# Optimization experiments

Measured on AMD Instinct MI355X. Metric: run time of the kernel, lower is better.

Reference implementation:

```python
import jax, jax.numpy as jnp
import numpy as np

B, T, HID = 2, 2048, 2048
NH, NKV = 16, 8
NOPE, ROPE = 128, 64
HD = NOPE + ROPE  # 192
VD = 128
KV_RANK, Q_RANK = 512, 1536
EPS = 1e-6
THETA = 10000.0
GROUPS = NH // NKV


def rmsnorm(x, w):
    var = jnp.mean(x * x, axis=-1, keepdims=True)
    return x * jax.lax.rsqrt(var + EPS) * w


def rope_cos_sin(seq_len, dtype):
    inv_freq = 1.0 / (THETA ** (jnp.arange(0, ROPE, 2, dtype=jnp.float32) / ROPE))
    t = jnp.arange(seq_len, dtype=jnp.float32)
    freqs = jnp.outer(t, inv_freq)
    emb = jnp.concatenate([freqs, freqs], axis=-1)  # [T, ROPE]
    return jnp.cos(emb).astype(dtype)[None, :, None, :], jnp.sin(emb).astype(dtype)[None, :, None, :]


def rotate_half(x):
    x1, x2 = x[..., : x.shape[-1] // 2], x[..., x.shape[-1] // 2 :]
    return jnp.concatenate([-x2, x1], axis=-1)


def setup_inputs() -> dict:
    key = jax.random.key(0)
    ks = jax.random.split(key, 7)
    s = 0.02
    return {
        "hidden_states": jax.random.normal(ks[0], (B, T, HID), jnp.float32),
        "q_a_w": jax.random.normal(ks[1], (HID, Q_RANK), jnp.float32) * s,
        "q_a_ln_w": jnp.ones((Q_RANK,), jnp.float32),
        "q_b_w": jax.random.normal(ks[2], (Q_RANK, NH * HD), jnp.float32) * s,
        "kv_a_w": jax.random.normal(ks[3], (HID, KV_RANK + NKV * ROPE), jnp.float32) * s,
        "kv_a_ln_w": jnp.ones((KV_RANK,), jnp.float32),
        "kv_b_w": jax.random.normal(ks[4], (KV_RANK, NKV * (NOPE + VD)), jnp.float32) * s,
        "o_w": jax.random.normal(ks[5], (NH * VD, HID), jnp.float32) * s,
    }


def reference(hidden_states, q_a_w, q_a_ln_w, q_b_w, kv_a_w, kv_a_ln_w, kv_b_w, o_w):
    x = hidden_states
    # Q low-rank path: a_proj -> RMSNorm -> b_proj
    q = rmsnorm(x @ q_a_w, q_a_ln_w) @ q_b_w
    q = q.reshape(B, T, NH, HD)
    q_nope, q_rope = q[..., :NOPE], q[..., NOPE:]
    # KV low-rank + decoupled rope key
    kv_raw = x @ kv_a_w
    kv_latent = rmsnorm(kv_raw[..., :KV_RANK], kv_a_ln_w)
    k_rope = kv_raw[..., KV_RANK:].reshape(B, T, NKV, ROPE)
    kv = (kv_latent @ kv_b_w).reshape(B, T, NKV, NOPE + VD)
    k_nope, v = kv[..., :NOPE], kv[..., NOPE:]
    # partial RoPE on rope slice only
    cos, sin = rope_cos_sin(T, x.dtype)
    q_rope = q_rope * cos + rotate_half(q_rope) * sin
    k_rope = k_rope * cos + rotate_half(k_rope) * sin
    q_full = jnp.concatenate([q_nope, q_rope], axis=-1)  # [B,T,NH,HD]
    k_full = jnp.concatenate([k_nope, k_rope], axis=-1)  # [B,T,NKV,HD]
    # GQA expansion (repeat_interleave over head dim)
    k_full = jnp.repeat(k_full, GROUPS, axis=2)  # [B,T,NH,HD]
    v_full = jnp.repeat(v, GROUPS, axis=2)       # [B,T,NH,VD]
    scale = HD ** -0.5
    scores = jnp.einsum("bqhd,bkhd->bhqk", q_full, k_full) * scale
    probs = jax.nn.softmax(scores, axis=-1)
    attn = jnp.einsum("bhqk,bkhd->bqhd", probs, v_full)
    out = attn.reshape(B, T, NH * VD) @ o_w
    return out
```

## Files before the change

kernel.cpp:

```cpp
#include <hip/hip_runtime.h>

using u16 = unsigned short;
using u32 = unsigned int;

typedef float f32x4 __attribute__((ext_vector_type(4)));
typedef __bf16 bf16x8 __attribute__((ext_vector_type(8)));

__device__ __forceinline__ u16 f2bf(float f){
  u32 u = __builtin_bit_cast(u32, f);
  u32 r = (u + 0x7fffu + ((u >> 16) & 1u)) >> 16;
  return (u16)r;
}
__device__ __forceinline__ float bf2f(u16 h){
  u32 u = ((u32)h) << 16;
  return __builtin_bit_cast(float, u);
}
__device__ __forceinline__ void gl2lds16(const void* g, void* l){
  __builtin_amdgcn_global_load_lds((const __attribute__((address_space(1))) u32*)g,
                                   (__attribute__((address_space(3))) u32*)l, 16, 0, 0);
}
__device__ __forceinline__ int swz24(int ck, int r){ return (ck & 24) | ((ck ^ r) & 7); }
__device__ __forceinline__ u32 cvtpk_bf16(float a, float b){
  u32 r; asm("v_cvt_pk_bf16_f32 %0, %1, %2" : "=v"(r) : "v"(a), "v"(b)); return r;
}

__global__ __launch_bounds__(256) void cvt_f32_bf16(const float* __restrict__ in,
                                                    u16* __restrict__ out, long n){
  long i = ((long)blockIdx.x*256 + threadIdx.x)*4;
  if (i >= n) return;
  float4 v = *(const float4*)(in + i);
  u16 o[4] = { f2bf(v.x), f2bf(v.y), f2bf(v.z), f2bf(v.w) };
  *(ushort4*)(out + i) = *(ushort4*)o;
}

__global__ __launch_bounds__(256) void transpose_w(const float* __restrict__ in,
                                                   u16* __restrict__ out, int K, int N){
  __shared__ float tile[32][33];
  int n0 = blockIdx.x*32, k0 = blockIdx.y*32;
  int tx = threadIdx.x, ty = threadIdx.y;
  for (int i = ty; i < 32; i += 8)
    tile[i][tx] = in[(size_t)(k0+i)*N + n0+tx];
  __syncthreads();
  for (int i = ty; i < 32; i += 8)
    out[(size_t)(n0+i)*K + k0+tx] = f2bf(tile[tx][i]);
}

__global__ __launch_bounds__(256) void rope_tables(float* __restrict__ cosT, float* __restrict__ sinT){
  int idx = blockIdx.x*256 + threadIdx.x;
  int t = idx >> 5, d = idx & 31;
  double inv = pow(10000.0, -(double)d / 32.0);
  double a = (double)t * inv;
  cosT[idx] = (float)cos(a);
  sinT[idx] = (float)sin(a);
}

__device__ __forceinline__ void remap_block(int NX, int& bx, int& by){
  int id = blockIdx.y*NX + blockIdx.x;
  bx = id >> 5;
  by = ((id & 7) << 2) | ((id >> 3) & 3);
}

template<int OUT_BF16>
__global__ __launch_bounds__(256) void gemm_bt(const u16* __restrict__ A,
                                               const u16* __restrict__ Bt,
                                               void* __restrict__ Cout,
                                               int M, int N, int K, float cscale){
  __shared__ u16 As[128*32];
  __shared__ u16 Bs[128*32];
  const int tid = threadIdx.x, lane = tid & 63, wave = tid >> 6;
  int bx, by; remap_block(gridDim.x, bx, by);
  const int m0 = by*128, n0 = bx*128;
  const int wm = (wave >> 1)*64, wn = (wave & 1)*64;
  const int g = lane >> 4, lr = lane & 15;
  f32x4 acc[4][4] = {};
  const int sr = (wave*2)*16 + (lane >> 2);
  const int sc = (lane & 3)*8;
  for (int k0 = 0; k0 < K; k0 += 32){
    __syncthreads();
    #pragma unroll
    for (int i = 0; i < 2; i++){
      int c = wave*2 + i;
      int r = sr + i*16;
      gl2lds16(A  + (size_t)(m0+r)*K + k0 + sc, (char*)As + c*1024);
      gl2lds16(Bt + (size_t)(n0+r)*K + k0 + sc, (char*)Bs + c*1024);
    }
    __syncthreads();
    bf16x8 af[4], bfr[4];
    #pragma unroll
    for (int mi = 0; mi < 4; mi++) af[mi]  = *reinterpret_cast<const bf16x8*>(&As[(wm+mi*16+lr)*32 + g*8]);
    #pragma unroll
    for (int ni = 0; ni < 4; ni++) bfr[ni] = *reinterpret_cast<const bf16x8*>(&Bs[(wn+ni*16+lr)*32 + g*8]);
    #pragma unroll
    for (int mi = 0; mi < 4; mi++)
      #pragma unroll
      for (int ni = 0; ni < 4; ni++)
        acc[mi][ni] = __builtin_amdgcn_mfma_f32_16x16x32_bf16(af[mi], bfr[ni], acc[mi][ni], 0,0,0);
  }
  #pragma unroll
  for (int mi = 0; mi < 4; mi++)
    #pragma unroll
    for (int ni = 0; ni < 4; ni++)
      #pragma unroll
      for (int r = 0; r < 4; r++){
        int row = m0 + wm + mi*16 + g*4 + r;
        int col = n0 + wn + ni*16 + lr;
        float v = acc[mi][ni][r];
        if (OUT_BF16) ((u16*)Cout)[(size_t)row*N + col] = f2bf(v*cscale);
        else          ((float*)Cout)[(size_t)row*N + col] = v;
      }
}

__global__ __launch_bounds__(256) void gemm_qb_rope(const u16* __restrict__ A,
                                                    const u16* __restrict__ Bt,
                                                    u16* __restrict__ C,
                                                    const float* __restrict__ cosT,
                                                    const float* __restrict__ sinT){
  constexpr int N = 3072, K = 1536;
  constexpr float qscale = 0.07216878364870322f;
  __shared__ u16 As[128*32];
  __shared__ u16 Bs[128*32];
  const int tid = threadIdx.x, lane = tid & 63, wave = tid >> 6;
  int bx, by; remap_block(gridDim.x, bx, by);
  const int m0 = by*128, n0 = bx*128;
  const int wm = (wave >> 1)*64, wn = (wave & 1)*64;
  const int g = lane >> 4, lr = lane & 15;
  f32x4 acc[4][4] = {};
  const int sr = (wave*2)*16 + (lane >> 2);
  const int sc = (lane & 3)*8;
  for (int k0 = 0; k0 < K; k0 += 32){
    __syncthreads();
    #pragma unroll
    for (int i = 0; i < 2; i++){
      int c = wave*2 + i;
      int r = sr + i*16;
      gl2lds16(A  + (size_t)(m0+r)*K + k0 + sc, (char*)As + c*1024);
      gl2lds16(Bt + (size_t)(n0+r)*K + k0 + sc, (char*)Bs + c*1024);
    }
    __syncthreads();
    bf16x8 af[4], bfr[4];
    #pragma unroll
    for (int mi = 0; mi < 4; mi++) af[mi]  = *reinterpret_cast<const bf16x8*>(&As[(wm+mi*16+lr)*32 + g*8]);
    #pragma unroll
    for (int ni = 0; ni < 4; ni++) bfr[ni] = *reinterpret_cast<const bf16x8*>(&Bs[(wn+ni*16+lr)*32 + g*8]);
    #pragma unroll
    for (int mi = 0; mi < 4; mi++)
      #pragma unroll
      for (int ni = 0; ni < 4; ni++)
        acc[mi][ni] = __builtin_amdgcn_mfma_f32_16x16x32_bf16(af[mi], bfr[ni], acc[mi][ni], 0,0,0);
  }
  const bool rope = (((n0 + wn) >> 6) % 3) == 2;
  #pragma unroll
  for (int mi = 0; mi < 4; mi++)
    #pragma unroll
    for (int r = 0; r < 4; r++){
      int row = m0 + wm + mi*16 + g*4 + r;
      int t = row & 2047;
      u16* crow = C + (size_t)row*N + n0 + wn;
      if (rope){
        #pragma unroll
        for (int np = 0; np < 2; np++){
          int dp = np*16 + lr;
          float x1 = acc[mi][np][r]*qscale, x2 = acc[mi][np+2][r]*qscale;
          float cv = cosT[t*32 + dp], sv = sinT[t*32 + dp];
          crow[dp]      = f2bf(x1*cv - x2*sv);
          crow[dp + 32] = f2bf(x2*cv + x1*sv);
        }
      } else {
        #pragma unroll
        for (int ni = 0; ni < 4; ni++)
          crow[ni*16 + lr] = f2bf(acc[mi][ni][r]*qscale);
      }
    }
}

__global__ __launch_bounds__(256) void rmsnorm_bf16(const u16* __restrict__ in,
                                                    const float* __restrict__ w,
                                                    u16* __restrict__ out, int ncols, int instride){
  int row = blockIdx.x;
  const u16* x = in + (size_t)row*instride;
  int c = threadIdx.x;
  float xs[8];
  float ss = 0.f;
  int nch = ncols >> 3;
  if (c < nch){
    ushort4 a = *(const ushort4*)(x + c*8);
    ushort4 bq = *(const ushort4*)(x + c*8 + 4);
    u16 e[8] = {a.x,a.y,a.z,a.w,bq.x,bq.y,bq.z,bq.w};
    #pragma unroll
    for (int j = 0; j < 8; j++){ xs[j] = bf2f(e[j]); ss += xs[j]*xs[j]; }
  }
  #pragma unroll
  for (int m = 1; m < 64; m <<= 1) ss += __shfl_xor(ss, m, 64);
  __shared__ float p[4];
  if ((threadIdx.x & 63) == 0) p[threadIdx.x >> 6] = ss;
  __syncthreads();
  float inv = rsqrtf((p[0]+p[1]+p[2]+p[3]) / (float)ncols + 1e-6f);
  if (c < nch){
    u16 o[8];
    #pragma unroll
    for (int j = 0; j < 8; j++) o[j] = f2bf(xs[j]*inv*w[c*8+j]);
    *(ushort4*)(out + (size_t)row*ncols + c*8)     = *(ushort4*)o;
    *(ushort4*)(out + (size_t)row*ncols + c*8 + 4) = *(ushort4*)(o+4);
  }
}

__global__ __launch_bounds__(256) void kv_split_kernel(const u16* __restrict__ kvraw,
                                                       const float* __restrict__ lnw,
                                                       const float* __restrict__ cosT,
                                                       const float* __restrict__ sinT,
                                                       u16* __restrict__ kvlat,
                                                       u16* __restrict__ Kf){
  int row = blockIdx.x;
  int t = row & 2047, b = row >> 11;
  const u16* x = kvraw + (size_t)row*2560 + 1536;
  int c = threadIdx.x;
  float xs[4];
  float ss = 0.f;
  if (c < 128){
    ushort4 a = *(const ushort4*)(x + c*4);
    u16 e[4] = {a.x,a.y,a.z,a.w};
    #pragma unroll
    for (int j = 0; j < 4; j++){ xs[j] = bf2f(e[j]); ss += xs[j]*xs[j]; }
  }
  #pragma unroll
  for (int m = 1; m < 64; m <<= 1) ss += __shfl_xor(ss, m, 64);
  __shared__ float p[4];
  if ((threadIdx.x & 63) == 0) p[threadIdx.x >> 6] = ss;
  __syncthreads();
  float inv = rsqrtf((p[0]+p[1]+p[2]+p[3]) / 512.0f + 1e-6f);
  if (c < 128){
    u16 o[4];
    #pragma unroll
    for (int j = 0; j < 4; j++) o[j] = f2bf(xs[j]*inv*lnw[c*4+j]);
    *(ushort4*)(kvlat + (size_t)row*512 + c*4) = *(ushort4*)o;
  }
  int kh = threadIdx.x >> 5, dp = threadIdx.x & 31;
  float x1 = bf2f(x[512 + kh*64 + dp]), x2 = bf2f(x[512 + kh*64 + dp + 32]);
  float cv = cosT[t*32 + dp], sv = sinT[t*32 + dp];
  float o1 = x1*cv - x2*sv;
  float o2 = x2*cv + x1*sv;
  u16* kr = Kf + ((size_t)(b*8 + kh)*2048 + t)*192;
  int c1 = 128 + dp, c2 = 128 + dp + 32;
  kr[(swz24(c1 >> 3, t) << 3) | (c1 & 7)] = f2bf(o1);
  kr[(swz24(c2 >> 3, t) << 3) | (c2 & 7)] = f2bf(o2);
}

__global__ __launch_bounds__(256) void kv_rearrange(const u16* __restrict__ kv,
                                                    u16* __restrict__ vT,
                                                    u16* __restrict__ Kf){
  int bid = blockIdx.x;
  int tt = bid & 31, kvh = (bid >> 5) & 7, b = bid >> 8;
  int t0 = tt*64;
  __shared__ u16 tile[64][136];
  int tid = threadIdx.x;
  #pragma unroll
  for (int i = 0; i < 4; i++){
    int c2 = tid + i*256;
    int rr = c2 >> 4, ck = c2 & 15;
    int t = t0 + rr;
    int ck2 = (ck & 8) | ((ck ^ t) & 7);
    uint4 v = *(const uint4*)(kv + ((size_t)(b*2048 + t))*2048 + kvh*256 + ck*8);
    *(uint4*)(Kf + ((size_t)(b*8 + kvh)*2048 + t)*192 + ck2*8) = v;
  }
  #pragma unroll
  for (int i = 0; i < 4; i++){
    int c = tid + i*256;
    int r = c >> 4, ck = c & 15;
    const u16* src = kv + ((size_t)(b*2048 + t0 + r))*2048 + kvh*256 + 128 + ck*8;
    *(uint4*)&tile[r][ck*8] = *(const uint4*)src;
  }
  __syncthreads();
  #pragma unroll
  for (int i = 0; i < 4; i++){
    int c = tid + i*256;
    int vd = c >> 3, tc = c & 7;
    int stc = tc ^ (vd & 7);
    uint4 tv;
    u16* tp = (u16*)&tv;
    #pragma unroll
    for (int j = 0; j < 8; j++) tp[j] = tile[tc*8 + j][vd];
    *(uint4*)(vT + ((size_t)(b*8 + kvh)*128 + vd)*2048 + t0 + stc*8) = tv;
  }
}

__global__ __launch_bounds__(256, 2) void attn_kernel(const u16* __restrict__ Q,
                                                      const u16* __restrict__ Kf,
                                                      const u16* __restrict__ Vt,
                                                      u16* __restrict__ Oa){
  constexpr int T = 2048;
  constexpr int NT = T/64;
  __shared__ u16 Ks[64*192];
  __shared__ u16 Vs[2][128*64];
  __shared__ u16 Ps[4][2048];
  const int tid = threadIdx.x, lane = tid & 63, wave = tid >> 6;
  const int g = lane >> 4, lr = lane & 15;

  const int wg = blockIdx.x;
  const int role = (wg & 7)*64 + (wg >> 3);
  const int grp = role >> 5;
  const int b = grp >> 3, kvh = grp & 7;
  const int within = role & 31;
  const int h = kvh*2 + (within >> 4);
  const int q0 = (within & 15)*128 + wave*32;

  bf16x8 aq[2][6];
  #pragma unroll
  for (int qg = 0; qg < 2; qg++){
    const u16* qrow = Q + ((size_t)b*T + q0 + qg*16 + lr)*3072 + h*192;
    #pragma unroll
    for (int kc = 0; kc < 6; kc++)
      aq[qg][kc] = *reinterpret_cast<const bf16x8*>(qrow + kc*32 + g*8);
  }
  const u16* Kbase = Kf + (size_t)(b*8 + kvh)*T*192;
  const u16* Vbase = Vt + (size_t)(b*8 + kvh)*128*T;

  f32x4 ovb[2][8] = {};
  float mq[2] = {-1e30f, -1e30f};
  float lq[2] = {0.f, 0.f};

  auto stageK = [&](int kt){
    const u16* ksrc = Kbase + (size_t)kt*12288 + wave*3072 + lane*8;
    #pragma unroll
    for (int i = 0; i < 6; i++)
      gl2lds16(ksrc + i*512, (char*)Ks + (wave*6 + i)*1024);
  };
  auto stageV = [&](int kt, int buf){
    #pragma unroll
    for (int i = 0; i < 4; i++){
      int c = wave*4 + i;
      const u16* vsrc = Vbase + (size_t)(c*8 + (lane >> 3))*T + kt*64 + (lane & 7)*8;
      gl2lds16(vsrc, (char*)(&Vs[0][0]) + buf*16384 + c*1024);
    }
  };

  stageK(0);
  stageV(0, 0);
  __syncthreads();

  int buf = 0;
  for (int kt = 0; kt < NT; kt++){
    const bool notlast = (kt + 1 < NT);
    if (notlast) stageV(kt + 1, buf ^ 1);

    f32x4 s[2][4];
    __builtin_amdgcn_s_setprio(1);
    #pragma unroll
    for (int nb = 0; nb < 4; nb++){
      const int row = nb*16 + lr;
      f32x4 a0 = {0.f,0.f,0.f,0.f}, a1 = {0.f,0.f,0.f,0.f};
      #pragma unroll
      for (int kc = 0; kc < 6; kc++){
        int ckl = swz24(kc*4 + g, row);
        bf16x8 kf = *reinterpret_cast<const bf16x8*>(&Ks[row*192 + ckl*8]);
        a0 = __builtin_amdgcn_mfma_f32_16x16x32_bf16(kf, aq[0][kc], a0, 0,0,0);
        a1 = __builtin_amdgcn_mfma_f32_16x16x32_bf16(kf, aq[1][kc], a1, 0,0,0);
      }
      s[0][nb] = a0; s[1][nb] = a1;
    }
    __builtin_amdgcn_s_setprio(0);

    asm volatile("s_waitcnt lgkmcnt(0)" ::: "memory");
    __builtin_amdgcn_s_barrier();
    __builtin_amdgcn_sched_barrier(0);
    if (notlast) stageK(kt + 1);

    #pragma unroll
    for (int qg = 0; qg < 2; qg++){
      float pm = s[qg][0][0];
      #pragma unroll
      for (int nb = 0; nb < 4; nb++)
        #pragma unroll
        for (int r = 0; r < 4; r++)
          if (nb || r) pm = fmaxf(pm, s[qg][nb][r]);
      pm = fmaxf(pm, __shfl_xor(pm, 16, 64));
      pm = fmaxf(pm, __shfl_xor(pm, 32, 64));
      if (!__all(pm <= mq[qg] + 8.f)){
        float mn = fmaxf(mq[qg], pm);
        float corr = __expf(mq[qg] - mn);
        mq[qg] = mn;
        lq[qg] *= corr;
        #pragma unroll
        for (int r = 0; r < 4; r++){
          float cr = __shfl(corr, (lane & 48) | (g*4 + r), 64);
          #pragma unroll
          for (int vb = 0; vb < 8; vb++) ovb[qg][vb][r] *= cr;
        }
      }
      float ls = 0.f;
      #pragma unroll
      for (int nb = 0; nb < 4; nb++){
        float e0 = __expf(s[qg][nb][0] - mq[qg]);
        float e1 = __expf(s[qg][nb][1] - mq[qg]);
        float e2 = __expf(s[qg][nb][2] - mq[qg]);
        float e3 = __expf(s[qg][nb][3] - mq[qg]);
        ls += (e0 + e1) + (e2 + e3);
        int stc = (2*nb + (g >> 1)) ^ (lr & 7);
        volatile u32* p = (volatile u32*)&Ps[wave][qg*1024 + lr*64 + stc*8 + (g & 1)*4];
        p[0] = cvtpk_bf16(e0, e1);
        p[1] = cvtpk_bf16(e2, e3);
      }
      ls += __shfl_xor(ls, 16, 64);
      ls += __shfl_xor(ls, 32, 64);
      lq[qg] += ls;
    }

    asm volatile("s_waitcnt lgkmcnt(0)" ::: "memory");
    __builtin_amdgcn_sched_barrier(0);

    bf16x8 ap[2][2];
    #pragma unroll
    for (int qg = 0; qg < 2; qg++)
      #pragma unroll
      for (int k2 = 0; k2 < 2; k2++){
        int ck = (k2*4 + g) ^ (lr & 7);
        ap[qg][k2] = *reinterpret_cast<const bf16x8*>(&Ps[wave][qg*1024 + lr*64 + ck*8]);
      }
    __builtin_amdgcn_s_setprio(1);
    #pragma unroll
    for (int vb = 0; vb < 8; vb++)
      #pragma unroll
      for (int k2 = 0; k2 < 2; k2++){
        int vd = vb*16 + lr;
        int ck = (k2*4 + g) ^ (vd & 7);
        bf16x8 bv = *reinterpret_cast<const bf16x8*>(&Vs[buf][vd*64 + ck*8]);
        ovb[0][vb] = __builtin_amdgcn_mfma_f32_16x16x32_bf16(ap[0][k2], bv, ovb[0][vb], 0,0,0);
        ovb[1][vb] = __builtin_amdgcn_mfma_f32_16x16x32_bf16(ap[1][k2], bv, ovb[1][vb], 0,0,0);
      }
    __builtin_amdgcn_s_setprio(0);

    if (notlast) __syncthreads();
    buf ^= 1;
  }

  #pragma unroll
  for (int qg = 0; qg < 2; qg++){
    float invq = 1.0f / lq[qg];
    float inv_r[4];
    #pragma unroll
    for (int r = 0; r < 4; r++)
      inv_r[r] = __shfl(invq, (lane & 48) | (g*4 + r), 64);
    u16* obase = Oa + ((size_t)b*T + q0 + qg*16)*2048 + h*128;
    #pragma unroll
    for (int vb = 0; vb < 8; vb++)
      #pragma unroll
      for (int r = 0; r < 4; r++)
        obase[(size_t)(g*4 + r)*2048 + vb*16 + lr] = f2bf(ovb[qg][vb][r]*inv_r[r]);
  }
}

extern "C" void kernel_launch(void* const* d_in, const int* in_sizes, int n_in,
                              void* d_out, int out_size, void* d_ws, size_t ws_size,
                              hipStream_t stream){
  const float* hs      = (const float*)d_in[0];
  const float* q_a_w   = (const float*)d_in[1];
  const float* q_a_ln  = (const float*)d_in[2];
  const float* q_b_w   = (const float*)d_in[3];
  const float* kv_a_w  = (const float*)d_in[4];
  const float* kv_a_ln = (const float*)d_in[5];
  const float* kv_b_w  = (const float*)d_in[6];
  const float* o_w     = (const float*)d_in[7];

  char* ws = (char*)d_ws;
  size_t off = 0;
  auto alloc = [&](size_t bytes){ void* p = ws + off; off += bytes; return p; };
  u16*  Wqa   = (u16*)alloc(1536ull*2048*2);
  u16*  Wkva  = (u16*)alloc(1024ull*2048*2);
  u16*  Wqb   = (u16*)alloc(3072ull*1536*2);
  u16*  Wkvb  = (u16*)alloc(2048ull*512*2);
  u16*  Wo    = (u16*)alloc(2048ull*2048*2);
  u16*  XB    = (u16*)alloc(4096ull*2048*2);
  u16*  R23   = (u16*)alloc(4096ull*2560*2);
  u16*  QB    = (u16*)alloc(4096ull*3072*2);
  u16*  Qlat  = (u16*)alloc(4096ull*1536*2);
  u16*  KVlat = (u16*)alloc(4096ull*512*2);
  u16*  Kf    = (u16*)alloc(2ull*8*2048*192*2);
  u16*  Vt    = (u16*)alloc(2ull*8*128*2048*2);
  float* cosT = (float*)alloc(2048ull*32*4);
  float* sinT = (float*)alloc(2048ull*32*4);
  (void)ws_size; (void)in_sizes; (void)n_in; (void)out_size;

  u16* KVB = R23;

  cvt_f32_bf16<<<8192, 256, 0, stream>>>(hs, XB, 4096ll*2048);
  transpose_w<<<dim3(1536/32, 2048/32), dim3(32,8), 0, stream>>>(q_a_w,  Wqa,  2048, 1536);
  transpose_w<<<dim3(1024/32, 2048/32), dim3(32,8), 0, stream>>>(kv_a_w, Wkva, 2048, 1024);
  transpose_w<<<dim3(3072/32, 1536/32), dim3(32,8), 0, stream>>>(q_b_w,  Wqb,  1536, 3072);
  transpose_w<<<dim3(2048/32,  512/32), dim3(32,8), 0, stream>>>(kv_b_w, Wkvb,  512, 2048);
  transpose_w<<<dim3(2048/32, 2048/32), dim3(32,8), 0, stream>>>(o_w,    Wo,   2048, 2048);
  rope_tables<<<256, 256, 0, stream>>>(cosT, sinT);

  gemm_bt<1><<<dim3(20, 32), 256, 0, stream>>>(XB, Wqa, R23, 4096, 2560, 2048, 1.0f);
  rmsnorm_bf16<<<4096, 256, 0, stream>>>(R23, q_a_ln, Qlat, 1536, 2560);
  kv_split_kernel<<<4096, 256, 0, stream>>>(R23, kv_a_ln, cosT, sinT, KVlat, Kf);
  gemm_qb_rope<<<dim3(24, 32), 256, 0, stream>>>(Qlat, Wqb, QB, cosT, sinT);
  gemm_bt<1><<<dim3(16, 32), 256, 0, stream>>>(KVlat, Wkvb, KVB, 4096, 2048, 512, 1.0f);
  kv_rearrange<<<512, 256, 0, stream>>>(KVB, Vt, Kf);
  attn_kernel<<<512, 256, 0, stream>>>(QB, Kf, Vt, XB);
  gemm_bt<0><<<dim3(16, 32), 256, 0, stream>>>(XB, Wo, (float*)d_out, 4096, 2048, 2048, 1.0f);
}
```

Measured before the change: 348.5 us.

## Pass P via shuffles, single-buffer V, use exp2 with folded log2e, raise occupancy

The attention kernel stops staging softmax probabilities through LDS and builds the MFMA A-operands with cross-lane shuffles instead. It drops the V double buffer, so V for the next tile is loaded only after a barrier at the end of each iteration. The freed LDS allows launch bounds of three blocks per SM. log2(e) is folded into the Q scale so exp2f can replace __expf, and the row-sum reduction is deferred to the epilogue. The risk is that V load latency is now exposed and the shuffle work may cost more than the LDS round trip it replaces.

```diff
diff --git a/kernel.cpp b/kernel.cpp
--- a/kernel.cpp
+++ b/kernel.cpp
@@ -5,6 +5,7 @@
 
 typedef float f32x4 __attribute__((ext_vector_type(4)));
 typedef __bf16 bf16x8 __attribute__((ext_vector_type(8)));
+typedef u32 u32x4 __attribute__((ext_vector_type(4)));
 
 __device__ __forceinline__ u16 f2bf(float f){
   u32 u = __builtin_bit_cast(u32, f);
@@ -116,7 +117,7 @@
                                                     const float* __restrict__ cosT,
                                                     const float* __restrict__ sinT){
   constexpr int N = 3072, K = 1536;
-  constexpr float qscale = 0.07216878364870322f;
+  constexpr float qscale = 0.07216878364870322f * 1.44269504088896340f;
   __shared__ u16 As[128*32];
   __shared__ u16 Bs[128*32];
   const int tid = threadIdx.x, lane = tid & 63, wave = tid >> 6;
@@ -283,15 +284,14 @@
   }
 }
 
-__global__ __launch_bounds__(256, 2) void attn_kernel(const u16* __restrict__ Q,
+__global__ __launch_bounds__(256, 3) void attn_kernel(const u16* __restrict__ Q,
                                                       const u16* __restrict__ Kf,
                                                       const u16* __restrict__ Vt,
                                                       u16* __restrict__ Oa){
   constexpr int T = 2048;
   constexpr int NT = T/64;
   __shared__ u16 Ks[64*192];
-  __shared__ u16 Vs[2][128*64];
-  __shared__ u16 Ps[4][2048];
+  __shared__ u16 Vs[128*64];
   const int tid = threadIdx.x, lane = tid & 63, wave = tid >> 6;
   const int g = lane >> 4, lr = lane & 15;
 
@@ -324,23 +324,21 @@
     for (int i = 0; i < 6; i++)
       gl2lds16(ksrc + i*512, (char*)Ks + (wave*6 + i)*1024);
   };
-  auto stageV = [&](int kt, int buf){
+  auto stageV = [&](int kt){
     #pragma unroll
     for (int i = 0; i < 4; i++){
       int c = wave*4 + i;
       const u16* vsrc = Vbase + (size_t)(c*8 + (lane >> 3))*T + kt*64 + (lane & 7)*8;
-      gl2lds16(vsrc, (char*)(&Vs[0][0]) + buf*16384 + c*1024);
+      gl2lds16(vsrc, (char*)Vs + c*1024);
     }
   };
 
   stageK(0);
-  stageV(0, 0);
+  stageV(0);
   __syncthreads();
 
-  int buf = 0;
   for (int kt = 0; kt < NT; kt++){
     const bool notlast = (kt + 1 < NT);
-    if (notlast) stageV(kt + 1, buf ^ 1);
 
     f32x4 s[2][4];
     __builtin_amdgcn_s_setprio(1);
@@ -359,11 +357,10 @@
     }
     __builtin_amdgcn_s_setprio(0);
 
-    asm volatile("s_waitcnt lgkmcnt(0)" ::: "memory");
-    __builtin_amdgcn_s_barrier();
-    __builtin_amdgcn_sched_barrier(0);
+    __syncthreads();
     if (notlast) stageK(kt + 1);
 
+    u32 pk[2][4][2];
     #pragma unroll
     for (int qg = 0; qg < 2; qg++){
       float pm = s[qg][0][0];
@@ -376,7 +373,7 @@
       pm = fmaxf(pm, __shfl_xor(pm, 32, 64));
       if (!__all(pm <= mq[qg] + 8.f)){
         float mn = fmaxf(mq[qg], pm);
-        float corr = __expf(mq[qg] - mn);
+        float corr = exp2f(mq[qg] - mn);
         mq[qg] = mn;
         lq[qg] *= corr;
         #pragma unroll
@@ -389,52 +386,64 @@
       float ls = 0.f;
       #pragma unroll
       for (int nb = 0; nb < 4; nb++){
-        float e0 = __expf(s[qg][nb][0] - mq[qg]);
-        float e1 = __expf(s[qg][nb][1] - mq[qg]);
-        float e2 = __expf(s[qg][nb][2] - mq[qg]);
-        float e3 = __expf(s[qg][nb][3] - mq[qg]);
+        float e0 = exp2f(s[qg][nb][0] - mq[qg]);
+        float e1 = exp2f(s[qg][nb][1] - mq[qg]);
+        float e2 = exp2f(s[qg][nb][2] - mq[qg]);
+        float e3 = exp2f(s[qg][nb][3] - mq[qg]);
         ls += (e0 + e1) + (e2 + e3);
-        int stc = (2*nb + (g >> 1)) ^ (lr & 7);
-        volatile u32* p = (volatile u32*)&Ps[wave][qg*1024 + lr*64 + stc*8 + (g & 1)*4];
-        p[0] = cvtpk_bf16(e0, e1);
-        p[1] = cvtpk_bf16(e2, e3);
-      }
-      ls += __shfl_xor(ls, 16, 64);
-      ls += __shfl_xor(ls, 32, 64);
+        pk[qg][nb][0] = cvtpk_bf16(e0, e1);
+        pk[qg][nb][1] = cvtpk_bf16(e2, e3);
+      }
       lq[qg] += ls;
     }
 
-    asm volatile("s_waitcnt lgkmcnt(0)" ::: "memory");
-    __builtin_amdgcn_sched_barrier(0);
-
-    bf16x8 ap[2][2];
-    #pragma unroll
-    for (int qg = 0; qg < 2; qg++)
-      #pragma unroll
-      for (int k2 = 0; k2 < 2; k2++){
-        int ck = (k2*4 + g) ^ (lr & 7);
-        ap[qg][k2] = *reinterpret_cast<const bf16x8*>(&Ps[wave][qg*1024 + lr*64 + ck*8]);
-      }
-    __builtin_amdgcn_s_setprio(1);
-    #pragma unroll
-    for (int vb = 0; vb < 8; vb++)
-      #pragma unroll
-      for (int k2 = 0; k2 < 2; k2++){
+    #pragma unroll
+    for (int c32 = 0; c32 < 2; c32++){
+      const int s0 = ((g & 1)*2)*16 + lr;
+      const int s1 = ((g & 1)*2 + 1)*16 + lr;
+      const int nbsel = g >> 1;
+      bf16x8 pa[2];
+      #pragma unroll
+      for (int qg = 0; qg < 2; qg++){
+        u32 a00 = (u32)__shfl((int)pk[qg][c32*2][0],   s0, 64);
+        u32 a01 = (u32)__shfl((int)pk[qg][c32*2][1],   s0, 64);
+        u32 a02 = (u32)__shfl((int)pk[qg][c32*2][0],   s1, 64);
+        u32 a03 = (u32)__shfl((int)pk[qg][c32*2][1],   s1, 64);
+        u32 a10 = (u32)__shfl((int)pk[qg][c32*2+1][0], s0, 64);
+        u32 a11 = (u32)__shfl((int)pk[qg][c32*2+1][1], s0, 64);
+        u32 a12 = (u32)__shfl((int)pk[qg][c32*2+1][0], s1, 64);
+        u32 a13 = (u32)__shfl((int)pk[qg][c32*2+1][1], s1, 64);
+        u32x4 av;
+        av.x = nbsel ? a10 : a00;
+        av.y = nbsel ? a11 : a01;
+        av.z = nbsel ? a12 : a02;
+        av.w = nbsel ? a13 : a03;
+        pa[qg] = __builtin_bit_cast(bf16x8, av);
+      }
+      __builtin_amdgcn_s_setprio(1);
+      #pragma unroll
+      for (int vb = 0; vb < 8; vb++){
         int vd = vb*16 + lr;
-        int ck = (k2*4 + g) ^ (vd & 7);
-        bf16x8 bv = *reinterpret_cast<const bf16x8*>(&Vs[buf][vd*64 + ck*8]);
-        ovb[0][vb] = __builtin_amdgcn_mfma_f32_16x16x32_bf16(ap[0][k2], bv, ovb[0][vb], 0,0,0);
-        ovb[1][vb] = __builtin_amdgcn_mfma_f32_16x16x32_bf16(ap[1][k2], bv, ovb[1][vb], 0,0,0);
-      }
-    __builtin_amdgcn_s_setprio(0);
-
-    if (notlast) __syncthreads();
-    buf ^= 1;
+        int ck = (c32*4 + g) ^ (vd & 7);
+        bf16x8 bv = *reinterpret_cast<const bf16x8*>(&Vs[vd*64 + ck*8]);
+        ovb[0][vb] = __builtin_amdgcn_mfma_f32_16x16x32_bf16(pa[0], bv, ovb[0][vb], 0,0,0);
+        ovb[1][vb] = __builtin_amdgcn_mfma_f32_16x16x32_bf16(pa[1], bv, ovb[1][vb], 0,0,0);
+      }
+      __builtin_amdgcn_s_setprio(0);
+    }
+
+    if (notlast){
+      __syncthreads();
+      stageV(kt + 1);
+    }
   }
 
   #pragma unroll
   for (int qg = 0; qg < 2; qg++){
-    float invq = 1.0f / lq[qg];
+    float lt = lq[qg];
+    lt += __shfl_xor(lt, 16, 64);
+    lt += __shfl_xor(lt, 32, 64);
+    float invq = 1.0f / lt;
     float inv_r[4];
     #pragma unroll
     for (int r = 0; r < 4; r++)
```

After: 432.5 us. 1.24x slower.

## Double-buffer GEMM LDS tiles and use exp2 softmax with deferred row-sum reduction

Applied to the files above, without the earlier changes.

The projection GEMMs now keep two LDS buffers, so the next K tile is fetched while the current one feeds the MFMAs, with one barrier per iteration instead of two. The attention softmax folds log2(e) into the Q scale so it can call exp2f instead of __expf. The cross-lane row-sum shuffles move out of the inner loop to a single reduction in the epilogue. The P-tile LDS swizzle also gains an extra XOR term meant to cut bank conflicts, at the cost of twice the LDS per GEMM block, which may lower occupancy.

```diff
diff --git a/kernel.cpp b/kernel.cpp
--- a/kernel.cpp
+++ b/kernel.cpp
@@ -65,8 +65,8 @@
                                                const u16* __restrict__ Bt,
                                                void* __restrict__ Cout,
                                                int M, int N, int K, float cscale){
-  __shared__ u16 As[128*32];
-  __shared__ u16 Bs[128*32];
+  __shared__ u16 As[2][128*32];
+  __shared__ u16 Bs[2][128*32];
   const int tid = threadIdx.x, lane = tid & 63, wave = tid >> 6;
   int bx, by; remap_block(gridDim.x, bx, by);
   const int m0 = by*128, n0 = bx*128;
@@ -75,26 +75,32 @@
   f32x4 acc[4][4] = {};
   const int sr = (wave*2)*16 + (lane >> 2);
   const int sc = (lane & 3)*8;
-  for (int k0 = 0; k0 < K; k0 += 32){
-    __syncthreads();
+  auto stage = [&](int k0, int bf){
     #pragma unroll
     for (int i = 0; i < 2; i++){
       int c = wave*2 + i;
       int r = sr + i*16;
-      gl2lds16(A  + (size_t)(m0+r)*K + k0 + sc, (char*)As + c*1024);
-      gl2lds16(Bt + (size_t)(n0+r)*K + k0 + sc, (char*)Bs + c*1024);
+      gl2lds16(A  + (size_t)(m0+r)*K + k0 + sc, (char*)(&As[bf][0]) + c*1024);
+      gl2lds16(Bt + (size_t)(n0+r)*K + k0 + sc, (char*)(&Bs[bf][0]) + c*1024);
     }
-    __syncthreads();
+  };
+  stage(0, 0);
+  __syncthreads();
+  int bf = 0;
+  for (int k0 = 0; k0 < K; k0 += 32){
+    if (k0 + 32 < K) stage(k0 + 32, bf ^ 1);
     bf16x8 af[4], bfr[4];
     #pragma unroll
-    for (int mi = 0; mi < 4; mi++) af[mi]  = *reinterpret_cast<const bf16x8*>(&As[(wm+mi*16+lr)*32 + g*8]);
-    #pragma unroll
-    for (int ni = 0; ni < 4; ni++) bfr[ni] = *reinterpret_cast<const bf16x8*>(&Bs[(wn+ni*16+lr)*32 + g*8]);
+    for (int mi = 0; mi < 4; mi++) af[mi]  = *reinterpret_cast<const bf16x8*>(&As[bf][(wm+mi*16+lr)*32 + g*8]);
+    #pragma unroll
+    for (int ni = 0; ni < 4; ni++) bfr[ni] = *reinterpret_cast<const bf16x8*>(&Bs[bf][(wn+ni*16+lr)*32 + g*8]);
     #pragma unroll
     for (int mi = 0; mi < 4; mi++)
       #pragma unroll
       for (int ni = 0; ni < 4; ni++)
         acc[mi][ni] = __builtin_amdgcn_mfma_f32_16x16x32_bf16(af[mi], bfr[ni], acc[mi][ni], 0,0,0);
+    __syncthreads();
+    bf ^= 1;
   }
   #pragma unroll
   for (int mi = 0; mi < 4; mi++)
@@ -116,9 +122,9 @@
                                                     const float* __restrict__ cosT,
                                                     const float* __restrict__ sinT){
   constexpr int N = 3072, K = 1536;
-  constexpr float qscale = 0.07216878364870322f;
-  __shared__ u16 As[128*32];
-  __shared__ u16 Bs[128*32];
+  constexpr float qscale = 0.07216878364870322f * 1.44269504088896340f;
+  __shared__ u16 As[2][128*32];
+  __shared__ u16 Bs[2][128*32];
   const int tid = threadIdx.x, lane = tid & 63, wave = tid >> 6;
   int bx, by; remap_block(gridDim.x, bx, by);
   const int m0 = by*128, n0 = bx*128;
@@ -127,26 +133,32 @@
   f32x4 acc[4][4] = {};
   const int sr = (wave*2)*16 + (lane >> 2);
   const int sc = (lane & 3)*8;
-  for (int k0 = 0; k0 < K; k0 += 32){
-    __syncthreads();
+  auto stage = [&](int k0, int bf){
     #pragma unroll
     for (int i = 0; i < 2; i++){
       int c = wave*2 + i;
       int r = sr + i*16;
-      gl2lds16(A  + (size_t)(m0+r)*K + k0 + sc, (char*)As + c*1024);
-      gl2lds16(Bt + (size_t)(n0+r)*K + k0 + sc, (char*)Bs + c*1024);
+      gl2lds16(A  + (size_t)(m0+r)*K + k0 + sc, (char*)(&As[bf][0]) + c*1024);
+      gl2lds16(Bt + (size_t)(n0+r)*K + k0 + sc, (char*)(&Bs[bf][0]) + c*1024);
     }
-    __syncthreads();
+  };
+  stage(0, 0);
+  __syncthreads();
+  int bf = 0;
+  for (int k0 = 0; k0 < K; k0 += 32){
+    if (k0 + 32 < K) stage(k0 + 32, bf ^ 1);
     bf16x8 af[4], bfr[4];
     #pragma unroll
-    for (int mi = 0; mi < 4; mi++) af[mi]  = *reinterpret_cast<const bf16x8*>(&As[(wm+mi*16+lr)*32 + g*8]);
-    #pragma unroll
-    for (int ni = 0; ni < 4; ni++) bfr[ni] = *reinterpret_cast<const bf16x8*>(&Bs[(wn+ni*16+lr)*32 + g*8]);
+    for (int mi = 0; mi < 4; mi++) af[mi]  = *reinterpret_cast<const bf16x8*>(&As[bf][(wm+mi*16+lr)*32 + g*8]);
+    #pragma unroll
+    for (int ni = 0; ni < 4; ni++) bfr[ni] = *reinterpret_cast<const bf16x8*>(&Bs[bf][(wn+ni*16+lr)*32 + g*8]);
     #pragma unroll
     for (int mi = 0; mi < 4; mi++)
       #pragma unroll
       for (int ni = 0; ni < 4; ni++)
         acc[mi][ni] = __builtin_amdgcn_mfma_f32_16x16x32_bf16(af[mi], bfr[ni], acc[mi][ni], 0,0,0);
+    __syncthreads();
+    bf ^= 1;
   }
   const bool rope = (((n0 + wn) >> 6) % 3) == 2;
   #pragma unroll
@@ -376,7 +388,7 @@
       pm = fmaxf(pm, __shfl_xor(pm, 32, 64));
       if (!__all(pm <= mq[qg] + 8.f)){
         float mn = fmaxf(mq[qg], pm);
-        float corr = __expf(mq[qg] - mn);
+        float corr = exp2f(mq[qg] - mn);
         mq[qg] = mn;
         lq[qg] *= corr;
         #pragma unroll
@@ -389,18 +401,16 @@
       float ls = 0.f;
       #pragma unroll
       for (int nb = 0; nb < 4; nb++){
-        float e0 = __expf(s[qg][nb][0] - mq[qg]);
-        float e1 = __expf(s[qg][nb][1] - mq[qg]);
-        float e2 = __expf(s[qg][nb][2] - mq[qg]);
-        float e3 = __expf(s[qg][nb][3] - mq[qg]);
+        float e0 = exp2f(s[qg][nb][0] - mq[qg]);
+        float e1 = exp2f(s[qg][nb][1] - mq[qg]);
+        float e2 = exp2f(s[qg][nb][2] - mq[qg]);
+        float e3 = exp2f(s[qg][nb][3] - mq[qg]);
         ls += (e0 + e1) + (e2 + e3);
-        int stc = (2*nb + (g >> 1)) ^ (lr & 7);
+        int stc = ((2*nb + (g >> 1)) ^ (lr & 7)) ^ ((lr >> 3) << 2);
         volatile u32* p = (volatile u32*)&Ps[wave][qg*1024 + lr*64 + stc*8 + (g & 1)*4];
         p[0] = cvtpk_bf16(e0, e1);
         p[1] = cvtpk_bf16(e2, e3);
       }
-      ls += __shfl_xor(ls, 16, 64);
-      ls += __shfl_xor(ls, 32, 64);
       lq[qg] += ls;
     }
 
@@ -412,7 +422,7 @@
     for (int qg = 0; qg < 2; qg++)
       #pragma unroll
       for (int k2 = 0; k2 < 2; k2++){
-        int ck = (k2*4 + g) ^ (lr & 7);
+        int ck = ((k2*4 + g) ^ (lr & 7)) ^ ((lr >> 3) << 2);
         ap[qg][k2] = *reinterpret_cast<const bf16x8*>(&Ps[wave][qg*1024 + lr*64 + ck*8]);
       }
     __builtin_amdgcn_s_setprio(1);
@@ -434,7 +444,10 @@
 
   #pragma unroll
   for (int qg = 0; qg < 2; qg++){
-    float invq = 1.0f / lq[qg];
+    float lt = lq[qg];
+    lt += __shfl_xor(lt, 16, 64);
+    lt += __shfl_xor(lt, 32, 64);
+    float invq = 1.0f / lt;
     float inv_r[4];
     #pragma unroll
     for (int r = 0; r < 4; r++)
```

Result: slower. 369.5 us (+6.0%).

## Share K/V tiles across both GQA heads in 512-thread attention blocks

Applied to the files above, without the earlier changes.

The attention kernel now runs 512-thread blocks in which waves 0-3 handle one query head and waves 4-7 the other head of the same KV group. Each K/V tile staged into shared memory therefore serves both heads, which halves global-to-LDS traffic per head. The log2(e) factor is folded into the Q scale so exp2f replaces __expf. The per-tile cross-lane row-sum reduction is deferred to the epilogue. The larger block doubles the P scratch buffer and raises per-block register and LDS pressure, which could limit occupancy.

```diff
diff --git a/kernel.cpp b/kernel.cpp
--- a/kernel.cpp
+++ b/kernel.cpp
@@ -116,7 +116,7 @@
                                                     const float* __restrict__ cosT,
                                                     const float* __restrict__ sinT){
   constexpr int N = 3072, K = 1536;
-  constexpr float qscale = 0.07216878364870322f;
+  constexpr float qscale = 0.07216878364870322f * 1.44269504088896340f;
   __shared__ u16 As[128*32];
   __shared__ u16 Bs[128*32];
   const int tid = threadIdx.x, lane = tid & 63, wave = tid >> 6;
@@ -283,7 +283,7 @@
   }
 }
 
-__global__ __launch_bounds__(256, 2) void attn_kernel(const u16* __restrict__ Q,
+__global__ __launch_bounds__(512, 2) void attn_kernel(const u16* __restrict__ Q,
                                                       const u16* __restrict__ Kf,
                                                       const u16* __restrict__ Vt,
                                                       u16* __restrict__ Oa){
@@ -291,17 +291,17 @@
   constexpr int NT = T/64;
   __shared__ u16 Ks[64*192];
   __shared__ u16 Vs[2][128*64];
-  __shared__ u16 Ps[4][2048];
+  __shared__ u16 Ps[8][2048];
   const int tid = threadIdx.x, lane = tid & 63, wave = tid >> 6;
   const int g = lane >> 4, lr = lane & 15;
 
   const int wg = blockIdx.x;
-  const int role = (wg & 7)*64 + (wg >> 3);
-  const int grp = role >> 5;
+  const int role = (wg & 7)*32 + (wg >> 3);
+  const int grp = role >> 4;
   const int b = grp >> 3, kvh = grp & 7;
-  const int within = role & 31;
-  const int h = kvh*2 + (within >> 4);
-  const int q0 = (within & 15)*128 + wave*32;
+  const int qtile = role & 15;
+  const int h = kvh*2 + (wave >> 2);
+  const int q0 = qtile*128 + (wave & 3)*32;
 
   bf16x8 aq[2][6];
   #pragma unroll
@@ -319,15 +319,16 @@
   float lq[2] = {0.f, 0.f};
 
   auto stageK = [&](int kt){
-    const u16* ksrc = Kbase + (size_t)kt*12288 + wave*3072 + lane*8;
-    #pragma unroll
-    for (int i = 0; i < 6; i++)
-      gl2lds16(ksrc + i*512, (char*)Ks + (wave*6 + i)*1024);
+    #pragma unroll
+    for (int i = 0; i < 3; i++){
+      int c = wave*3 + i;
+      gl2lds16(Kbase + (size_t)kt*12288 + c*512 + lane*8, (char*)Ks + c*1024);
+    }
   };
   auto stageV = [&](int kt, int buf){
     #pragma unroll
-    for (int i = 0; i < 4; i++){
-      int c = wave*4 + i;
+    for (int i = 0; i < 2; i++){
+      int c = wave*2 + i;
       const u16* vsrc = Vbase + (size_t)(c*8 + (lane >> 3))*T + kt*64 + (lane & 7)*8;
       gl2lds16(vsrc, (char*)(&Vs[0][0]) + buf*16384 + c*1024);
     }
@@ -376,7 +377,7 @@
       pm = fmaxf(pm, __shfl_xor(pm, 32, 64));
       if (!__all(pm <= mq[qg] + 8.f)){
         float mn = fmaxf(mq[qg], pm);
-        float corr = __expf(mq[qg] - mn);
+        float corr = exp2f(mq[qg] - mn);
         mq[qg] = mn;
         lq[qg] *= corr;
         #pragma unroll
@@ -389,18 +390,16 @@
       float ls = 0.f;
       #pragma unroll
       for (int nb = 0; nb < 4; nb++){
-        float e0 = __expf(s[qg][nb][0] - mq[qg]);
-        float e1 = __expf(s[qg][nb][1] - mq[qg]);
-        float e2 = __expf(s[qg][nb][2] - mq[qg]);
-        float e3 = __expf(s[qg][nb][3] - mq[qg]);
+        float e0 = exp2f(s[qg][nb][0] - mq[qg]);
+        float e1 = exp2f(s[qg][nb][1] - mq[qg]);
+        float e2 = exp2f(s[qg][nb][2] - mq[qg]);
+        float e3 = exp2f(s[qg][nb][3] - mq[qg]);
         ls += (e0 + e1) + (e2 + e3);
         int stc = (2*nb + (g >> 1)) ^ (lr & 7);
         volatile u32* p = (volatile u32*)&Ps[wave][qg*1024 + lr*64 + stc*8 + (g & 1)*4];
         p[0] = cvtpk_bf16(e0, e1);
         p[1] = cvtpk_bf16(e2, e3);
       }
-      ls += __shfl_xor(ls, 16, 64);
-      ls += __shfl_xor(ls, 32, 64);
       lq[qg] += ls;
     }
 
@@ -434,7 +433,10 @@
 
   #pragma unroll
   for (int qg = 0; qg < 2; qg++){
-    float invq = 1.0f / lq[qg];
+    float lt = lq[qg];
+    lt += __shfl_xor(lt, 16, 64);
+    lt += __shfl_xor(lt, 32, 64);
+    float invq = 1.0f / lt;
     float inv_r[4];
     #pragma unroll
     for (int r = 0; r < 4; r++)
@@ -495,6 +497,6 @@
   gemm_qb_rope<<<dim3(24, 32), 256, 0, stream>>>(Qlat, Wqb, QB, cosT, sinT);
   gemm_bt<1><<<dim3(16, 32), 256, 0, stream>>>(KVlat, Wkvb, KVB, 4096, 2048, 512, 1.0f);
   kv_rearrange<<<512, 256, 0, stream>>>(KVB, Vt, Kf);
-  attn_kernel<<<512, 256, 0, stream>>>(QB, Kf, Vt, XB);
+  attn_kernel<<<256, 512, 0, stream>>>(QB, Kf, Vt, XB);
   gemm_bt<0><<<dim3(16, 32), 256, 0, stream>>>(XB, Wo, (float*)d_out, 4096, 2048, 2048, 1.0f);
 }
```

New measurement: 361.0 us. 3.6% more time.
